# Optimization experiments

Measured on AMD Instinct MI355X. Metric: run time of the kernel, lower is better.

Reference implementation:

```python
import jax, jax.numpy as jnp
import numpy as np

N = 100_000        # nodes
E = 1_600_000      # edges (avg degree 16)
NODE_DIM = 64
HIDDEN = 64
OUT = 32


def _glorot(key, fan_in, fan_out):
    lim = np.sqrt(6.0 / (fan_in + fan_out)).astype(np.float32)
    return jax.random.uniform(key, (fan_in, fan_out), jnp.float32, -lim, lim)


def setup_inputs() -> dict:
    key = jax.random.key(0)
    ks = jax.random.split(key, 5)
    x = jax.random.normal(ks[0], (N, NODE_DIM), jnp.float32)
    edge_index = jax.random.randint(ks[1], (2, E), 0, N, dtype=jnp.int64)
    return {
        "x": x,
        "edge_index": edge_index,
        "W1": _glorot(ks[2], NODE_DIM, HIDDEN),
        "b1": jnp.zeros((HIDDEN,), jnp.float32),
        "Wmu": _glorot(ks[3], HIDDEN, OUT),
        "bmu": jnp.zeros((OUT,), jnp.float32),
        "Wlv": _glorot(ks[4], HIDDEN, OUT),
        "blv": jnp.zeros((OUT,), jnp.float32),
    }


def _gcn_conv(h, W, b, src, dst, norm, n):
    """PyG GCNConv: linear (no bias) -> normalized scatter-add -> + bias.
    src/dst/norm already include self-loops and deg^{-1/2} symmetric norm."""
    h = h @ W                                   # [n, out]
    msg = h[src] * norm[:, None]                # [E+N, out] gather
    out = jax.ops.segment_sum(msg, dst, num_segments=n)  # scatter-add
    return out + b


def reference(x, edge_index, W1, b1, Wmu, bmu, Wlv, blv):
    loops = jnp.arange(N, dtype=edge_index.dtype)
    src = jnp.concatenate([edge_index[0], loops])  # add self-loops
    dst = jnp.concatenate([edge_index[1], loops])
    # symmetric normalization: deg computed on target nodes (all weights 1)
    deg = jax.ops.segment_sum(jnp.ones_like(src, dtype=x.dtype), dst, num_segments=N)
    dinv = jax.lax.rsqrt(deg)                   # deg >= 1 due to self-loops
    norm = dinv[src] * dinv[dst]

    h = jax.nn.relu(_gcn_conv(x, W1, b1, src, dst, norm, N))
    mu = _gcn_conv(h, Wmu, bmu, src, dst, norm, N)
    logvar = _gcn_conv(h, Wlv, blv, src, dst, norm, N)
    return mu, logvar
```

## Files before the change

### kernel.cpp

```cpp
#include <hip/hip_runtime.h>
#include <hip/hip_fp16.h>


#define BKT_SHIFT 9
#define BKT_NODES 512
#define CHUNK 8192

typedef __attribute__((ext_vector_type(8))) _Float16 half8;
typedef __attribute__((ext_vector_type(4))) float float4v;
typedef __attribute__((ext_vector_type(4))) unsigned uint4v;

__device__ __forceinline__ int imin(int a, int b) { return a < b ? a : b; }
__device__ __forceinline__ int imax(int a, int b) { return a > b ? a : b; }
__device__ __forceinline__ unsigned h2u(__half2 v) {
  union { __half2 h; unsigned u; } c; c.h = v; return c.u;
}
__device__ __forceinline__ __half2 u2h(unsigned x) {
  union { unsigned u; __half2 h; } c; c.u = x; return c.h;
}


__global__ __launch_bounds__(1024) void block_sums(const int* __restrict__ in,
                                                   int* __restrict__ bsum, int n) {
  __shared__ int s[1024];
  int t = threadIdx.x;
  int i = blockIdx.x * 1024 + t;
  s[t] = (i < n) ? in[i] : 0;
  __syncthreads();
  for (int off = 512; off > 0; off >>= 1) {
    if (t < off) s[t] += s[t + off];
    __syncthreads();
  }
  if (t == 0) bsum[blockIdx.x] = s[0];
}

__global__ __launch_bounds__(1024) void scan_bsums(int* __restrict__ bsum, int nb) {
  __shared__ int s[1024];
  int t = threadIdx.x;
  int v = (t < nb) ? bsum[t] : 0;
  s[t] = v;
  __syncthreads();
  for (int off = 1; off < 1024; off <<= 1) {
    int u = (t >= off) ? s[t - off] : 0;
    __syncthreads();
    s[t] += u;
    __syncthreads();
  }
  if (t < nb) bsum[t] = s[t] - v;
}

__global__ __launch_bounds__(1024) void scan_apply(int* __restrict__ data,
                                                   const int* __restrict__ bofs, int n) {
  __shared__ int s[1024];
  int t = threadIdx.x;
  int i = blockIdx.x * 1024 + t;
  int c = (i < n) ? data[i] : 0;
  s[t] = c;
  __syncthreads();
  for (int off = 1; off < 1024; off <<= 1) {
    int u = (t >= off) ? s[t - off] : 0;
    __syncthreads();
    s[t] += u;
    __syncthreads();
  }
  if (i < n) data[i] = bofs[blockIdx.x] + s[t] - c;
}


__global__ __launch_bounds__(256) void bucket_count(const int* __restrict__ dst,
                                                    int* __restrict__ cnt,
                                                    int E, int nbk, int nblk) {
  __shared__ int hist[256];
  int t = threadIdx.x;
  hist[t] = 0;
  __syncthreads();
  int base = blockIdx.x * CHUNK;
  int end = imin(base + CHUNK, E);
  for (int e = base + t; e < end; e += 256) atomicAdd(&hist[dst[e] >> BKT_SHIFT], 1);
  __syncthreads();
  if (t < nbk) cnt[t * nblk + blockIdx.x] = hist[t];
}

__global__ __launch_bounds__(256) void bucket_scatter(const int* __restrict__ src,
                                                      const int* __restrict__ dst,
                                                      const int* __restrict__ ofs,
                                                      int2* __restrict__ tmp,
                                                      int E, int nbk, int nblk) {
  __shared__ int cur[256];
  int t = threadIdx.x;
  if (t < nbk) cur[t] = ofs[t * nblk + blockIdx.x];
  __syncthreads();
  int base = blockIdx.x * CHUNK;
  int end = imin(base + CHUNK, E);
  for (int e = base + t; e < end; e += 256) {
    int d = dst[e];
    int pos = atomicAdd(&cur[d >> BKT_SHIFT], 1);
    tmp[pos] = make_int2(src[e], d);
  }
}

__global__ __launch_bounds__(512) void bucket_build(const int2* __restrict__ tmp,
                                                    const int* __restrict__ ofs,
                                                    int* __restrict__ row_ptr,
                                                    float* __restrict__ dinv,
                                                    int* __restrict__ pairs,
                                                    int n, int nbk, int nblk, int E) {
  __shared__ int hist[BKT_NODES];
  __shared__ int scn[BKT_NODES];
  const int b = blockIdx.x;
  const int t = threadIdx.x;
  const int node0 = b << BKT_SHIFT;
  hist[t] = 0;
  __syncthreads();
  const int s = ofs[b * nblk];
  const int e = (b + 1 < nbk) ? ofs[(b + 1) * nblk] : E;
  for (int k = s + t; k < e; k += 512) atomicAdd(&hist[tmp[k].y - node0], 1);
  __syncthreads();
  int v = hist[t];
  scn[t] = v;
  __syncthreads();
  for (int off = 1; off < 512; off <<= 1) {
    int u = (t >= off) ? scn[t - off] : 0;
    __syncthreads();
    scn[t] += u;
    __syncthreads();
  }
  int excl = s + scn[t] - v;
  int node = node0 + t;
  if (node < n) {
    row_ptr[node] = excl;
    dinv[node] = rsqrtf(1.0f + (float)v);
  }
  if (b == nbk - 1 && t == 0) row_ptr[n] = E;
  hist[t] = excl;
  __syncthreads();
  for (int k = s + t; k < e; k += 512) {
    int2 p = tmp[k];
    int pos = atomicAdd(&hist[p.y - node0], 1);
    pairs[pos] = p.x;
  }
}


__global__ __launch_bounds__(256) void cast_scale(const float* __restrict__ x,
                                                  const float* __restrict__ dinv,
                                                  __half* __restrict__ xs,
                                                  __half* __restrict__ hs,
                                                  int n4, int nrow) {
  int i = blockIdx.x * blockDim.x + threadIdx.x;
  if (i < n4) {
    float4 v = ((const float4*)x)[i];
    float d = dinv[i >> 4];
    __half2* o = (__half2*)(xs + (size_t)i * 4);
    o[0] = __floats2half2_rn(d * v.x, d * v.y);
    o[1] = __floats2half2_rn(d * v.z, d * v.w);
  } else if (i < n4 + 32) {
    int j = i - n4;
    if (j < 16)
      ((float2*)(xs + (size_t)nrow * 64))[j] = make_float2(0.f, 0.f);
    else
      ((float2*)(hs + (size_t)nrow * 64))[j - 16] = make_float2(0.f, 0.f);
  }
}


#define YSTRIDE 264

__global__ __launch_bounds__(256, 4) void agg_layer1(const __half* __restrict__ xs,
                                                     const int* __restrict__ pairs,
                                                     const int* __restrict__ row_ptr,
                                                     const float* __restrict__ W1,
                                                     const float* __restrict__ b1,
                                                     __half* __restrict__ hs, int n) {
  __shared__ _Float16 ylds_all[4][16 * YSTRIDE];
  __shared__ float dilds_all[4][16];
  const int wv = threadIdx.x >> 6;
  _Float16* ylds = ylds_all[wv];
  float* dilds = dilds_all[wv];
  const int lane = threadIdx.x & 63;
  const int g = lane >> 3, q = lane & 7;
  const int quad = lane >> 4, col = lane & 15;

  half8 bfrag[2][4];
#pragma unroll
  for (int s = 0; s < 2; ++s)
#pragma unroll
    for (int t = 0; t < 4; ++t)
#pragma unroll
      for (int jj = 0; jj < 8; ++jj)
        bfrag[s][t][jj] = (_Float16)W1[(s * 32 + quad * 8 + jj) * 64 + t * 16 + col];
  float bias[4];
#pragma unroll
  for (int t = 0; t < 4; ++t) bias[t] = b1[t * 16 + col];

  const int ntiles = (n + 15) >> 4;
  for (int tile = blockIdx.x * 4 + wv; tile < ntiles; tile += gridDim.x * 4) {
    const int row0 = tile << 4;
#pragma unroll 1
    for (int rg = 0; rg < 4; ++rg) {
      int start[4], end[4], idx[4];
      __half2 acc[4][4];
      int maxdeg = 0;
#pragma unroll
      for (int j = 0; j < 4; ++j) {
        const int i = row0 + rg * 4 + j;
        start[j] = 0; end[j] = 0;
        if (i < n) { start[j] = row_ptr[i]; end[j] = row_ptr[i + 1]; }
        maxdeg = imax(maxdeg, end[j] - start[j]);
#pragma unroll
        for (int k = 0; k < 4; ++k) acc[j][k] = u2h(0u);
        idx[j] = (start[j] + g < end[j]) ? pairs[start[j] + g] : n;
      }
      const int iters = (maxdeg + 7) >> 3;
#pragma unroll 1
      for (int it = 0; it < iters; ++it) {
        int nidx[4];
#pragma unroll
        for (int j = 0; j < 4; ++j) {
          const int ofs = start[j] + (it + 1) * 8 + g;
          nidx[j] = (ofs < end[j]) ? pairs[ofs] : n;
        }
#pragma unroll
        for (int j = 0; j < 4; ++j) {
          const float4 rr = *(const float4*)(xs + (size_t)idx[j] * 64 + q * 8);
          const __half2* hp = (const __half2*)&rr;
#pragma unroll
          for (int k = 0; k < 4; ++k) acc[j][k] = __hadd2(acc[j][k], hp[k]);
        }
#pragma unroll
        for (int j = 0; j < 4; ++j) idx[j] = nidx[j];
      }
#pragma unroll
      for (int j = 0; j < 4; ++j) {
        const int i = row0 + rg * 4 + j;
        if (g == 0 && i < n) {
          const float4 sr = *(const float4*)(xs + (size_t)i * 64 + q * 8);
          const __half2* hp = (const __half2*)&sr;
#pragma unroll
          for (int k = 0; k < 4; ++k) acc[j][k] = __hadd2(acc[j][k], hp[k]);
        }
#pragma unroll
        for (int k = 0; k < 4; ++k) {
          unsigned u = __shfl_xor(h2u(acc[j][k]), 32);
          acc[j][k] = __hadd2(acc[j][k], u2h(u));
        }
        const float di = rsqrtf((float)(1 + end[j] - start[j]));
        const __half hdi = __float2half(di);
        const __half2 di2 = __halves2half2(hdi, hdi);
        uint4v st;
        st.x = h2u(__hmul2(di2, acc[j][0]));
        st.y = h2u(__hmul2(di2, acc[j][1]));
        st.z = h2u(__hmul2(di2, acc[j][2]));
        st.w = h2u(__hmul2(di2, acc[j][3]));
        *(uint4v*)(ylds + (rg * 4 + j) * YSTRIDE + (g & 3) * 64 + q * 8) = st;
        if (lane == 0) dilds[rg * 4 + j] = di;
      }
    }
    float4v acc[4];
#pragma unroll
    for (int t = 0; t < 4; ++t) acc[t] = (float4v){bias[t], bias[t], bias[t], bias[t]};
#pragma unroll
    for (int s2 = 0; s2 < 8; ++s2) {
      half8 af = *(half8*)(ylds + col * YSTRIDE + s2 * 32 + quad * 8);
      const int sW = s2 & 1;
#pragma unroll
      for (int t = 0; t < 4; ++t)
        acc[t] = __builtin_amdgcn_mfma_f32_16x16x32_f16(af, bfrag[sW][t], acc[t], 0, 0, 0);
    }
    const float4 dis = *(const float4*)(dilds + quad * 4);
    const float dd[4] = {dis.x, dis.y, dis.z, dis.w};
#pragma unroll
    for (int t = 0; t < 4; ++t)
#pragma unroll
      for (int reg = 0; reg < 4; ++reg) {
        const int row = row0 + quad * 4 + reg;
        if (row < n)
          hs[(size_t)row * 64 + t * 16 + col] =
              __float2half(dd[reg] * fmaxf(acc[t][reg], 0.f));
      }
  }
}

__global__ __launch_bounds__(256, 4) void agg_layer2(const __half* __restrict__ hsin,
                                                     const int* __restrict__ pairs,
                                                     const int* __restrict__ row_ptr,
                                                     const float* __restrict__ Wmu,
                                                     const float* __restrict__ bmu,
                                                     const float* __restrict__ Wlv,
                                                     const float* __restrict__ blv,
                                                     float* __restrict__ out_mu,
                                                     float* __restrict__ out_lv, int n) {
  __shared__ _Float16 ylds_all[4][16 * YSTRIDE];
  const int wv = threadIdx.x >> 6;
  _Float16* ylds = ylds_all[wv];
  const int lane = threadIdx.x & 63;
  const int g = lane >> 3, q = lane & 7;
  const int quad = lane >> 4, col = lane & 15;

  half8 bfrag[2][4];
#pragma unroll
  for (int s = 0; s < 2; ++s)
#pragma unroll
    for (int t = 0; t < 4; ++t) {
      const int j = t * 16 + col;
      const float* W = (j < 32) ? Wmu : Wlv;
      const int jc = j & 31;
#pragma unroll
      for (int jj = 0; jj < 8; ++jj)
        bfrag[s][t][jj] = (_Float16)W[(s * 32 + quad * 8 + jj) * 32 + jc];
    }
  float bias[4];
#pragma unroll
  for (int t = 0; t < 4; ++t) {
    const int j = t * 16 + col;
    bias[t] = (j < 32) ? bmu[j] : blv[j - 32];
  }

  const int ntiles = (n + 15) >> 4;
  for (int tile = blockIdx.x * 4 + wv; tile < ntiles; tile += gridDim.x * 4) {
    const int row0 = tile << 4;
#pragma unroll 1
    for (int rg = 0; rg < 4; ++rg) {
      int start[4], end[4], idx[4];
      __half2 acc[4][4];
      int maxdeg = 0;
#pragma unroll
      for (int j = 0; j < 4; ++j) {
        const int i = row0 + rg * 4 + j;
        start[j] = 0; end[j] = 0;
        if (i < n) { start[j] = row_ptr[i]; end[j] = row_ptr[i + 1]; }
        maxdeg = imax(maxdeg, end[j] - start[j]);
#pragma unroll
        for (int k = 0; k < 4; ++k) acc[j][k] = u2h(0u);
        idx[j] = (start[j] + g < end[j]) ? pairs[start[j] + g] : n;
      }
      const int iters = (maxdeg + 7) >> 3;
#pragma unroll 1
      for (int it = 0; it < iters; ++it) {
        int nidx[4];
#pragma unroll
        for (int j = 0; j < 4; ++j) {
          const int ofs = start[j] + (it + 1) * 8 + g;
          nidx[j] = (ofs < end[j]) ? pairs[ofs] : n;
        }
#pragma unroll
        for (int j = 0; j < 4; ++j) {
          const float4 rr = *(const float4*)(hsin + (size_t)idx[j] * 64 + q * 8);
          const __half2* hp = (const __half2*)&rr;
#pragma unroll
          for (int k = 0; k < 4; ++k) acc[j][k] = __hadd2(acc[j][k], hp[k]);
        }
#pragma unroll
        for (int j = 0; j < 4; ++j) idx[j] = nidx[j];
      }
#pragma unroll
      for (int j = 0; j < 4; ++j) {
        const int i = row0 + rg * 4 + j;
        if (g == 0 && i < n) {
          const float4 sr = *(const float4*)(hsin + (size_t)i * 64 + q * 8);
          const __half2* hp = (const __half2*)&sr;
#pragma unroll
          for (int k = 0; k < 4; ++k) acc[j][k] = __hadd2(acc[j][k], hp[k]);
        }
#pragma unroll
        for (int k = 0; k < 4; ++k) {
          unsigned u = __shfl_xor(h2u(acc[j][k]), 32);
          acc[j][k] = __hadd2(acc[j][k], u2h(u));
        }
        const float di = rsqrtf((float)(1 + end[j] - start[j]));
        const __half hdi = __float2half(di);
        const __half2 di2 = __halves2half2(hdi, hdi);
        uint4v st;
        st.x = h2u(__hmul2(di2, acc[j][0]));
        st.y = h2u(__hmul2(di2, acc[j][1]));
        st.z = h2u(__hmul2(di2, acc[j][2]));
        st.w = h2u(__hmul2(di2, acc[j][3]));
        *(uint4v*)(ylds + (rg * 4 + j) * YSTRIDE + (g & 3) * 64 + q * 8) = st;
      }
    }
    float4v acc[4];
#pragma unroll
    for (int t = 0; t < 4; ++t) acc[t] = (float4v){bias[t], bias[t], bias[t], bias[t]};
#pragma unroll
    for (int s2 = 0; s2 < 8; ++s2) {
      half8 af = *(half8*)(ylds + col * YSTRIDE + s2 * 32 + quad * 8);
      const int sW = s2 & 1;
#pragma unroll
      for (int t = 0; t < 4; ++t)
        acc[t] = __builtin_amdgcn_mfma_f32_16x16x32_f16(af, bfrag[sW][t], acc[t], 0, 0, 0);
    }
#pragma unroll
    for (int t = 0; t < 4; ++t)
#pragma unroll
      for (int reg = 0; reg < 4; ++reg) {
        const int row = row0 + quad * 4 + reg;
        if (row < n) {
          const int j = t * 16 + col;
          if (j < 32)
            out_mu[(size_t)row * 32 + j] = acc[t][reg];
          else
            out_lv[(size_t)row * 32 + (j - 32)] = acc[t][reg];
        }
      }
  }
}

extern "C" void kernel_launch(void* const* d_in, const int* in_sizes, int n_in,
                              void* d_out, int out_size, void* d_ws, size_t ws_size,
                              hipStream_t stream) {
  const float* x = (const float*)d_in[0];
  const int* ei = (const int*)d_in[1];
  const float* W1 = (const float*)d_in[2];
  const float* b1 = (const float*)d_in[3];
  const float* Wmu = (const float*)d_in[4];
  const float* bmu = (const float*)d_in[5];
  const float* Wlv = (const float*)d_in[6];
  const float* blv = (const float*)d_in[7];

  const int N = in_sizes[0] / 64;
  const int E = in_sizes[1] / 2;
  const int* src = ei;
  const int* dst = ei + E;

  const int NBK = (N + BKT_NODES - 1) >> BKT_SHIFT;
  const int NBLK = (E + CHUNK - 1) / CHUNK;
  const int FL = NBK * NBLK;

  auto align256 = [](size_t v) { return (v + 255) & ~(size_t)255; };
  char* p = (char*)d_ws;
  int* row_ptr = (int*)p;  p += align256((size_t)(N + 1) * 4);
  float* dinv = (float*)p; p += align256((size_t)N * 4);
  int* bsum = (int*)p;     p += align256((size_t)1024 * 4);
  int* cnt = (int*)p;      p += align256((size_t)FL * 4);
  int* pairs = (int*)p;    p += align256((size_t)E * 4);
  __half* xs = (__half*)p; p += align256((size_t)(N + 1) * 64 * 2);
  size_t tmp_bytes = (size_t)E * 8;
  size_t hs_bytes = (size_t)(N + 1) * 64 * 2;
  int2* tmp = (int2*)p;
  __half* hs = (__half*)p; p += align256(tmp_bytes > hs_bytes ? tmp_bytes : hs_bytes);

  float* out_mu = (float*)d_out;
  float* out_lv = out_mu + (size_t)N * 32;

  const int NB_F = (FL + 1023) / 1024;
  const int n4 = N * 16;

  bucket_count<<<NBLK, 256, 0, stream>>>(dst, cnt, E, NBK, NBLK);
  block_sums<<<NB_F, 1024, 0, stream>>>(cnt, bsum, FL);
  scan_bsums<<<1, 1024, 0, stream>>>(bsum, NB_F);
  scan_apply<<<NB_F, 1024, 0, stream>>>(cnt, bsum, FL);
  bucket_scatter<<<NBLK, 256, 0, stream>>>(src, dst, cnt, tmp, E, NBK, NBLK);
  bucket_build<<<NBK, 512, 0, stream>>>(tmp, cnt, row_ptr, dinv, pairs, N, NBK, NBLK, E);

  cast_scale<<<(n4 + 32 + 255) / 256, 256, 0, stream>>>(x, dinv, xs, hs, n4, N);

  const int ntiles = (N + 15) / 16;
  const int ablocks = (ntiles + 3) / 4;
  agg_layer1<<<ablocks, 256, 0, stream>>>(xs, pairs, row_ptr, W1, b1, hs, N);
  agg_layer2<<<ablocks, 256, 0, stream>>>(hs, pairs, row_ptr, Wmu, bmu, Wlv, blv,
                                          out_mu, out_lv, N);
}
```

Measured before the change: 253.4 us.

## Fuse cast-and-scale into bucket build and gather two neighbor batches per iteration

The separate cast_scale kernel is folded into bucket_build. Each bucket block now computes its nodes' deg^-1/2 in shared memory and writes the scaled fp16 feature rows directly, which removes a launch and the global dinv array. Both aggregation kernels now process 16 neighbors per loop iteration instead of 8, with two independent row loads per node. This puts more gathers in flight per iteration. The tradeoff is that the fused casting work runs on only about 196 large blocks, and the extra in-flight loads raise register pressure.

```diff
diff --git a/kernel.cpp b/kernel.cpp
--- a/kernel.cpp
+++ b/kernel.cpp
@@ -101,12 +101,15 @@
 
 __global__ __launch_bounds__(512) void bucket_build(const int2* __restrict__ tmp,
                                                     const int* __restrict__ ofs,
+                                                    const float* __restrict__ x,
                                                     int* __restrict__ row_ptr,
-                                                    float* __restrict__ dinv,
                                                     int* __restrict__ pairs,
+                                                    __half* __restrict__ xs,
+                                                    __half* __restrict__ hs,
                                                     int n, int nbk, int nblk, int E) {
   __shared__ int hist[BKT_NODES];
   __shared__ int scn[BKT_NODES];
+  __shared__ float dil[BKT_NODES];
   const int b = blockIdx.x;
   const int t = threadIdx.x;
   const int node0 = b << BKT_SHIFT;
@@ -116,7 +119,7 @@
   const int e = (b + 1 < nbk) ? ofs[(b + 1) * nblk] : E;
   for (int k = s + t; k < e; k += 512) atomicAdd(&hist[tmp[k].y - node0], 1);
   __syncthreads();
-  int v = hist[t];
+  const int v = hist[t];
   scn[t] = v;
   __syncthreads();
   for (int off = 1; off < 512; off <<= 1) {
@@ -125,12 +128,10 @@
     scn[t] += u;
     __syncthreads();
   }
-  int excl = s + scn[t] - v;
-  int node = node0 + t;
-  if (node < n) {
-    row_ptr[node] = excl;
-    dinv[node] = rsqrtf(1.0f + (float)v);
-  }
+  const int excl = s + scn[t] - v;
+  const int node = node0 + t;
+  if (node < n) row_ptr[node] = excl;
+  dil[t] = rsqrtf(1.0f + (float)v);
   if (b == nbk - 1 && t == 0) row_ptr[n] = E;
   hist[t] = excl;
   __syncthreads();
@@ -139,27 +140,22 @@
     int pos = atomicAdd(&hist[p.y - node0], 1);
     pairs[pos] = p.x;
   }
-}
-
-
-__global__ __launch_bounds__(256) void cast_scale(const float* __restrict__ x,
-                                                  const float* __restrict__ dinv,
-                                                  __half* __restrict__ xs,
-                                                  __half* __restrict__ hs,
-                                                  int n4, int nrow) {
-  int i = blockIdx.x * blockDim.x + threadIdx.x;
-  if (i < n4) {
-    float4 v = ((const float4*)x)[i];
-    float d = dinv[i >> 4];
-    __half2* o = (__half2*)(xs + (size_t)i * 4);
-    o[0] = __floats2half2_rn(d * v.x, d * v.y);
-    o[1] = __floats2half2_rn(d * v.z, d * v.w);
-  } else if (i < n4 + 32) {
-    int j = i - n4;
-    if (j < 16)
-      ((float2*)(xs + (size_t)nrow * 64))[j] = make_float2(0.f, 0.f);
+  const int nq = BKT_NODES * 16;
+  for (int k = t; k < nq; k += 512) {
+    const int nd = node0 + (k >> 4);
+    if (nd < n) {
+      const float4 vv = ((const float4*)x)[(size_t)nd * 16 + (k & 15)];
+      const float d = dil[k >> 4];
+      __half2* o = (__half2*)(xs + (size_t)nd * 64 + (k & 15) * 4);
+      o[0] = __floats2half2_rn(d * vv.x, d * vv.y);
+      o[1] = __floats2half2_rn(d * vv.z, d * vv.w);
+    }
+  }
+  if (b == 0 && t < 32) {
+    if (t < 16)
+      ((float2*)(xs + (size_t)n * 64))[t] = make_float2(0.f, 0.f);
     else
-      ((float2*)(hs + (size_t)nrow * 64))[j - 16] = make_float2(0.f, 0.f);
+      ((float2*)(hs + (size_t)n * 64))[t - 16] = make_float2(0.f, 0.f);
   }
 }
 
@@ -198,7 +194,7 @@
     const int row0 = tile << 4;
 #pragma unroll 1
     for (int rg = 0; rg < 4; ++rg) {
-      int start[4], end[4], idx[4];
+      int start[4], end[4], idx0[4], idx1[4];
       __half2 acc[4][4];
       int maxdeg = 0;
 #pragma unroll
@@ -209,26 +205,32 @@
         maxdeg = imax(maxdeg, end[j] - start[j]);
 #pragma unroll
         for (int k = 0; k < 4; ++k) acc[j][k] = u2h(0u);
-        idx[j] = (start[j] + g < end[j]) ? pairs[start[j] + g] : n;
-      }
-      const int iters = (maxdeg + 7) >> 3;
+        idx0[j] = (start[j] + g < end[j]) ? pairs[start[j] + g] : n;
+        idx1[j] = (start[j] + 8 + g < end[j]) ? pairs[start[j] + 8 + g] : n;
+      }
+      const int iters = (maxdeg + 15) >> 4;
 #pragma unroll 1
       for (int it = 0; it < iters; ++it) {
-        int nidx[4];
+        int nxt0[4], nxt1[4];
+        const int boff = (it + 1) * 16;
 #pragma unroll
         for (int j = 0; j < 4; ++j) {
-          const int ofs = start[j] + (it + 1) * 8 + g;
-          nidx[j] = (ofs < end[j]) ? pairs[ofs] : n;
+          const int o0 = start[j] + boff + g;
+          nxt0[j] = (o0 < end[j]) ? pairs[o0] : n;
+          nxt1[j] = (o0 + 8 < end[j]) ? pairs[o0 + 8] : n;
         }
 #pragma unroll
         for (int j = 0; j < 4; ++j) {
-          const float4 rr = *(const float4*)(xs + (size_t)idx[j] * 64 + q * 8);
-          const __half2* hp = (const __half2*)&rr;
-#pragma unroll
-          for (int k = 0; k < 4; ++k) acc[j][k] = __hadd2(acc[j][k], hp[k]);
-        }
-#pragma unroll
-        for (int j = 0; j < 4; ++j) idx[j] = nidx[j];
+          const float4 r0 = *(const float4*)(xs + (size_t)idx0[j] * 64 + q * 8);
+          const float4 r1 = *(const float4*)(xs + (size_t)idx1[j] * 64 + q * 8);
+          const __half2* h0 = (const __half2*)&r0;
+          const __half2* h1 = (const __half2*)&r1;
+#pragma unroll
+          for (int k = 0; k < 4; ++k)
+            acc[j][k] = __hadd2(__hadd2(acc[j][k], h0[k]), h1[k]);
+        }
+#pragma unroll
+        for (int j = 0; j < 4; ++j) { idx0[j] = nxt0[j]; idx1[j] = nxt1[j]; }
       }
 #pragma unroll
       for (int j = 0; j < 4; ++j) {
@@ -321,7 +323,7 @@
     const int row0 = tile << 4;
 #pragma unroll 1
     for (int rg = 0; rg < 4; ++rg) {
-      int start[4], end[4], idx[4];
+      int start[4], end[4], idx0[4], idx1[4];
       __half2 acc[4][4];
       int maxdeg = 0;
 #pragma unroll
@@ -332,26 +334,32 @@
         maxdeg = imax(maxdeg, end[j] - start[j]);
 #pragma unroll
         for (int k = 0; k < 4; ++k) acc[j][k] = u2h(0u);
-        idx[j] = (start[j] + g < end[j]) ? pairs[start[j] + g] : n;
-      }
-      const int iters = (maxdeg + 7) >> 3;
+        idx0[j] = (start[j] + g < end[j]) ? pairs[start[j] + g] : n;
+        idx1[j] = (start[j] + 8 + g < end[j]) ? pairs[start[j] + 8 + g] : n;
+      }
+      const int iters = (maxdeg + 15) >> 4;
 #pragma unroll 1
       for (int it = 0; it < iters; ++it) {
-        int nidx[4];
+        int nxt0[4], nxt1[4];
+        const int boff = (it + 1) * 16;
 #pragma unroll
         for (int j = 0; j < 4; ++j) {
-          const int ofs = start[j] + (it + 1) * 8 + g;
-          nidx[j] = (ofs < end[j]) ? pairs[ofs] : n;
+          const int o0 = start[j] + boff + g;
+          nxt0[j] = (o0 < end[j]) ? pairs[o0] : n;
+          nxt1[j] = (o0 + 8 < end[j]) ? pairs[o0 + 8] : n;
         }
 #pragma unroll
         for (int j = 0; j < 4; ++j) {
-          const float4 rr = *(const float4*)(hsin + (size_t)idx[j] * 64 + q * 8);
-          const __half2* hp = (const __half2*)&rr;
-#pragma unroll
-          for (int k = 0; k < 4; ++k) acc[j][k] = __hadd2(acc[j][k], hp[k]);
-        }
-#pragma unroll
-        for (int j = 0; j < 4; ++j) idx[j] = nidx[j];
+          const float4 r0 = *(const float4*)(hsin + (size_t)idx0[j] * 64 + q * 8);
+          const float4 r1 = *(const float4*)(hsin + (size_t)idx1[j] * 64 + q * 8);
+          const __half2* h0 = (const __half2*)&r0;
+          const __half2* h1 = (const __half2*)&r1;
+#pragma unroll
+          for (int k = 0; k < 4; ++k)
+            acc[j][k] = __hadd2(__hadd2(acc[j][k], h0[k]), h1[k]);
+        }
+#pragma unroll
+        for (int j = 0; j < 4; ++j) { idx0[j] = nxt0[j]; idx1[j] = nxt1[j]; }
       }
 #pragma unroll
       for (int j = 0; j < 4; ++j) {
@@ -429,7 +437,6 @@
   auto align256 = [](size_t v) { return (v + 255) & ~(size_t)255; };
   char* p = (char*)d_ws;
   int* row_ptr = (int*)p;  p += align256((size_t)(N + 1) * 4);
-  float* dinv = (float*)p; p += align256((size_t)N * 4);
   int* bsum = (int*)p;     p += align256((size_t)1024 * 4);
   int* cnt = (int*)p;      p += align256((size_t)FL * 4);
   int* pairs = (int*)p;    p += align256((size_t)E * 4);
@@ -437,22 +444,21 @@
   size_t tmp_bytes = (size_t)E * 8;
   size_t hs_bytes = (size_t)(N + 1) * 64 * 2;
   int2* tmp = (int2*)p;
-  __half* hs = (__half*)p; p += align256(tmp_bytes > hs_bytes ? tmp_bytes : hs_bytes);
+  __half* hs = (__half*)p;
+  p += align256(tmp_bytes > hs_bytes ? tmp_bytes : hs_bytes);
 
   float* out_mu = (float*)d_out;
   float* out_lv = out_mu + (size_t)N * 32;
 
   const int NB_F = (FL + 1023) / 1024;
-  const int n4 = N * 16;
 
   bucket_count<<<NBLK, 256, 0, stream>>>(dst, cnt, E, NBK, NBLK);
   block_sums<<<NB_F, 1024, 0, stream>>>(cnt, bsum, FL);
   scan_bsums<<<1, 1024, 0, stream>>>(bsum, NB_F);
   scan_apply<<<NB_F, 1024, 0, stream>>>(cnt, bsum, FL);
   bucket_scatter<<<NBLK, 256, 0, stream>>>(src, dst, cnt, tmp, E, NBK, NBLK);
-  bucket_build<<<NBK, 512, 0, stream>>>(tmp, cnt, row_ptr, dinv, pairs, N, NBK, NBLK, E);
-
-  cast_scale<<<(n4 + 32 + 255) / 256, 256, 0, stream>>>(x, dinv, xs, hs, n4, N);
+  bucket_build<<<NBK, 512, 0, stream>>>(tmp, cnt, x, row_ptr, pairs, xs, hs,
+                                        N, NBK, NBLK, E);
 
   const int ntiles = (N + 15) / 16;
   const int ablocks = (ntiles + 3) / 4;
```

Result: slower. 277.1 us (+9.4%).
